# Performance work log

Measured on AMD Instinct MI355X. Metric: run time of the kernel, lower is better.

Reference implementation:

```python
import jax, jax.numpy as jnp
import numpy as np

DN = ('NCHW', 'OIHW', 'NCHW')

def conv(x, w, b, stride, pad):
    y = jax.lax.conv_general_dilated(x, w, (stride, stride), ((pad, pad), (pad, pad)), dimension_numbers=DN)
    return y + b[None, :, None, None]

def conv_transpose(x, w, b, stride, pad):
    # w has torch ConvTranspose2d layout (Cin, Cout, kh, kw)
    k = w.shape[2]
    w_f = jnp.transpose(w[:, :, ::-1, ::-1], (1, 0, 2, 3))  # -> OIHW, spatially flipped
    p = k - 1 - pad
    y = jax.lax.conv_general_dilated(x, w_f, (1, 1), ((p, p), (p, p)), lhs_dilation=(stride, stride), dimension_numbers=DN)
    return y + b[None, :, None, None]

def setup_inputs() -> dict:
    key = jax.random.key(0)
    ks = jax.random.split(key, 16)
    K, D = 512, 64
    s = 0.05
    inp = {
        'x': jax.random.uniform(ks[0], (32, 3, 256, 256), dtype=jnp.float32),
        'enc_w1': jax.random.normal(ks[1], (32, 3, 4, 4), jnp.float32) * s,
        'enc_b1': jnp.zeros((32,), jnp.float32),
        'enc_w2': jax.random.normal(ks[2], (64, 32, 4, 4), jnp.float32) * s,
        'enc_b2': jnp.zeros((64,), jnp.float32),
        'enc_w3': jax.random.normal(ks[3], (D, 64, 3, 3), jnp.float32) * s,
        'enc_b3': jnp.zeros((D,), jnp.float32),
        'codebook': jax.random.uniform(ks[4], (K, D), jnp.float32, -1.0 / K, 1.0 / K),
        'dec_w1': jax.random.normal(ks[5], (D, 64, 4, 4), jnp.float32) * s,   # ConvT (Cin,Cout,k,k)
        'dec_b1': jnp.zeros((64,), jnp.float32),
        'dec_w2': jax.random.normal(ks[6], (64, 32, 4, 4), jnp.float32) * s,  # ConvT
        'dec_b2': jnp.zeros((32,), jnp.float32),
        'dec_w3': jax.random.normal(ks[7], (3, 32, 3, 3), jnp.float32) * s,
        'dec_b3': jnp.zeros((3,), jnp.float32),
    }
    return inp

COMMITMENT_COST = 0.25

def reference(x, enc_w1, enc_b1, enc_w2, enc_b2, enc_w3, enc_b3, codebook,
              dec_w1, dec_b1, dec_w2, dec_b2, dec_w3, dec_b3):
    sg = jax.lax.stop_gradient
    # encoder
    h = jax.nn.relu(conv(x, enc_w1, enc_b1, 2, 1))
    h = jax.nn.relu(conv(h, enc_w2, enc_b2, 2, 1))
    z = conv(h, enc_w3, enc_b3, 1, 1)  # [B, D, H/4, W/4]
    # vector quantizer
    D = codebook.shape[1]
    z_perm = jnp.transpose(z, (0, 2, 3, 1))  # BHWD
    flat = z_perm.reshape(-1, D)  # [N, D]
    dist = jnp.sum(flat * flat, axis=1, keepdims=True) - 2.0 * (flat @ codebook.T) + jnp.sum(codebook * codebook, axis=1)  # [N, K]
    idx = jnp.argmin(dist, axis=1)
    q = codebook[idx].reshape(z_perm.shape)
    q = jnp.transpose(q, (0, 3, 1, 2))  # BDHW
    vq_loss = jnp.mean((sg(q) - z) ** 2) + COMMITMENT_COST * jnp.mean((q - sg(z)) ** 2)
    q_st = z + sg(q - z)  # straight-through
    # decoder
    h = jax.nn.relu(conv_transpose(q_st, dec_w1, dec_b1, 2, 1))
    h = jax.nn.relu(conv_transpose(h, dec_w2, dec_b2, 2, 1))
    recon = jax.nn.sigmoid(conv(h, dec_w3, dec_b3, 1, 1))
    return recon, vq_loss
```

## Files before the change

kernel.cpp:

```cpp
#include <hip/hip_runtime.h>

typedef unsigned short u16;
typedef unsigned int u32;
typedef __attribute__((ext_vector_type(8))) short bf16x8;
typedef __attribute__((ext_vector_type(4))) float f32x4;

#define MFMA(a, b, c) __builtin_amdgcn_mfma_f32_16x16x32_bf16(a, b, c, 0, 0, 0)

__device__ __forceinline__ float b2f(u32 lo16) {
  union { u32 i; float f; } v; v.i = lo16 << 16; return v.f;
}
__device__ __forceinline__ u16 f2b(float f) {
  union { float f; u32 i; } v; v.f = f;
  return (u16)((v.i + 0x7fffu + ((v.i >> 16) & 1u)) >> 16);
}
__device__ __forceinline__ u32 pk2(float a, float b) {
  u32 r; asm("v_cvt_pk_bf16_f32 %0, %1, %2" : "=v"(r) : "v"(a), "v"(b)); return r;
}
__device__ __forceinline__ bf16x8 ld8(const u16* p) { return *(const bf16x8*)p; }

__global__ void prep_k(const float* __restrict__ ew1, const float* __restrict__ ew2,
                       const float* __restrict__ ew3, const float* __restrict__ dw1,
                       const float* __restrict__ dw2, const float* __restrict__ dw3,
                       const float* __restrict__ cb,
                       float* W1, u16* Bp2, u16* Bp3, u16* BpT1, u16* BpT2,
                       u16* Bpd3, u16* Bpvq, float* cnorm, float* loss) {
  int tid = blockIdx.x * blockDim.x + threadIdx.x;
  int nth = gridDim.x * blockDim.x;
  for (int i = tid; i < 1536; i += nth) {
    int oc = i & 31; int r = i >> 5; int kw = r & 3; r >>= 2; int kh = r & 3; int ic = r >> 2;
    W1[i] = ew1[((oc*3 + ic)*4 + kh)*4 + kw];
  }
  for (int i = tid; i < 32768; i += nth) {
    int j = i & 7, li = (i >> 3) & 63, nt = (i >> 9) & 3, t = i >> 11;
    int ic = 8*(li >> 4) + j, oc = 16*nt + (li & 15), kh = t >> 2, kw = t & 3;
    Bp2[i] = f2b(ew2[((oc*32 + ic)*4 + kh)*4 + kw]);
  }
  for (int i = tid; i < 36864; i += nth) {
    int j = i & 7, li = (i >> 3) & 63, nt = (i >> 9) & 3, kc = (i >> 11) & 1, t = i >> 12;
    int ic = 32*kc + 8*(li >> 4) + j, oc = 16*nt + (li & 15), kh = t / 3, kw = t % 3;
    Bp3[i] = f2b(ew3[((oc*64 + ic)*3 + kh)*3 + kw]);
  }
  for (int i = tid; i < 65536; i += nth) {
    int j = i & 7, li = (i >> 3) & 63, nt = (i >> 9) & 3, kc = (i >> 11) & 1,
        t = (i >> 12) & 3, p = i >> 14;
    int a = p >> 1, b = p & 1;
    int ky = (1 - a) + 2*(t >> 1), kx = (1 - b) + 2*(t & 1);
    int ic = 32*kc + 8*(li >> 4) + j, oc = 16*nt + (li & 15);
    BpT1[i] = f2b(dw1[((ic*64 + oc)*4 + ky)*4 + kx]);
  }
  for (int i = tid; i < 32768; i += nth) {
    int j = i & 7, li = (i >> 3) & 63, mt = (i >> 9) & 1, kc = (i >> 10) & 1,
        t = (i >> 11) & 3, p = i >> 13;
    int a = p >> 1, b = p & 1;
    int ky = (1 - a) + 2*(t >> 1), kx = (1 - b) + 2*(t & 1);
    int oc = 16*mt + (li & 15);
    int ic = 32*kc + 8*(li >> 4) + j;
    BpT2[i] = f2b(dw2[((ic*32 + oc)*4 + ky)*4 + kx]);
  }
  for (int i = tid; i < 4608; i += nth) {
    int j = i & 7, li = (i >> 3) & 63, t = i >> 9;
    int n = li & 15, ic = 8*(li >> 4) + j, kh = t / 3, kw = t % 3;
    Bpd3[i] = (n < 3) ? f2b(dw3[((n*32 + ic)*3 + kh)*3 + kw]) : (u16)0;
  }
  for (int i = tid; i < 32768; i += nth) {
    int j = i & 7, li = (i >> 3) & 63, nt = (i >> 9) & 31, kc = i >> 14;
    int d = 32*kc + 8*(li >> 4) + j, code = 16*nt + (li & 15);
    Bpvq[i] = f2b(cb[code*64 + d]);
  }
  for (int k = tid; k < 512; k += nth) {
    float s = 0.f;
    for (int d = 0; d < 64; ++d) { float c = cb[k*64 + d]; s += c*c; }
    cnorm[k] = s;
  }
  if (tid == 0) *loss = 0.f;
}

__global__ __launch_bounds__(256) void conv1_k(
    const float* __restrict__ x, const float* __restrict__ W1,
    const float* __restrict__ b1, u16* __restrict__ h1) {
  __shared__ float ins[3*18*36];
  int Tx = blockIdx.x, Ty = blockIdx.y, b = blockIdx.z;
  int tid = threadIdx.x;
  for (int i = tid; i < 3*18*36; i += 256) {
    int c = i % 36; int r = (i / 36) % 18; int ic = i / 648;
    int iy = 16*Ty - 1 + r, ix = 32*Tx - 2 + c;
    float v = 0.f;
    if ((unsigned)iy < 256u && (unsigned)ix < 256u)
      v = x[((size_t)(b*3 + ic)*256 + iy)*256 + ix];
    ins[i] = v;
  }
  __syncthreads();
  int posg = tid & 31, ocg = tid >> 5;
  int Y = posg >> 2, Xg = posg & 3;
  int oc0 = ocg * 4;
  float acc[4][4];
#pragma unroll
  for (int j = 0; j < 4; ++j) { float bv = b1[oc0 + j];
#pragma unroll
    for (int e = 0; e < 4; ++e) acc[j][e] = bv; }
  for (int ic = 0; ic < 3; ++ic)
#pragma unroll
    for (int kh = 0; kh < 4; ++kh) {
      const float* row = &ins[ic*648 + (2*Y + kh)*36 + 8*Xg];
      float win[12];
#pragma unroll
      for (int t = 0; t < 12; ++t) win[t] = row[t];
#pragma unroll
      for (int kw = 0; kw < 4; ++kw) {
        const float* wp = &W1[((ic*4 + kh)*4 + kw)*32 + oc0];
        float w0 = wp[0], w1 = wp[1], w2 = wp[2], w3 = wp[3];
#pragma unroll
        for (int e = 0; e < 4; ++e) {
          float v = win[2*e + kw + 1];
          acc[0][e] += w0*v; acc[1][e] += w1*v; acc[2][e] += w2*v; acc[3][e] += w3*v;
        }
      }
    }
  int oy = 8*Ty + Y;
  int oxb = 16*Tx + 4*Xg;
#pragma unroll
  for (int e = 0; e < 4; ++e) {
    u32 lo = pk2(fmaxf(acc[0][e], 0.f), fmaxf(acc[1][e], 0.f));
    u32 hi = pk2(fmaxf(acc[2][e], 0.f), fmaxf(acc[3][e], 0.f));
    *(uint2*)&h1[((size_t)(b*128 + oy)*128 + oxb + e)*32 + oc0] = (uint2){lo, hi};
  }
}

__global__ __launch_bounds__(256) void conv2_k(
    const u16* __restrict__ h1, const u16* __restrict__ Bp2,
    const float* __restrict__ eb2, u16* __restrict__ h2) {
  __shared__ u16 lds[2448*8];
  int Tx = blockIdx.x, Ty = blockIdx.y, img = blockIdx.z;
  int tid = threadIdx.x;
  for (int i = tid; i < 2448; i += 256) {
    int c = i & 3; int x = (i >> 2) % 34; int row = (i >> 2) / 34;
    int iy = 16*Ty - 1 + row, ix = 32*Tx - 1 + x;
    f32x4 v = {0,0,0,0};
    if ((unsigned)iy < 128u && (unsigned)ix < 128u)
      v = *(const f32x4*)(h1 + (((size_t)(img*128 + iy)*128 + ix)*32 + c*8));
    *(f32x4*)(lds + ((row*4 + c)*34 + x)*8) = v;
  }
  __syncthreads();
  int w = tid >> 6, l = tid & 63, lg = l >> 4, lc = l & 15;
  f32x4 acc[2][4];
#pragma unroll
  for (int mt = 0; mt < 4; ++mt) {
    f32x4 bv = *(const f32x4*)(eb2 + mt*16 + 4*lg);
    acc[0][mt] = bv; acc[1][mt] = bv;
  }
#pragma unroll
  for (int t = 0; t < 16; ++t) {
    int kh = t >> 2, kw = t & 3;
    bf16x8 a0 = ld8(lds + (((2*w + kh)*4 + lg)*34 + 2*lc + kw)*8);
    bf16x8 a1 = ld8(lds + (((2*(w+4) + kh)*4 + lg)*34 + 2*lc + kw)*8);
    const u16* bp = Bp2 + t*2048 + l*8;
    bf16x8 w0 = ld8(bp), w1 = ld8(bp + 512), w2 = ld8(bp + 1024), w3 = ld8(bp + 1536);
    acc[0][0] = MFMA(w0, a0, acc[0][0]); acc[0][1] = MFMA(w1, a0, acc[0][1]);
    acc[0][2] = MFMA(w2, a0, acc[0][2]); acc[0][3] = MFMA(w3, a0, acc[0][3]);
    acc[1][0] = MFMA(w0, a1, acc[1][0]); acc[1][1] = MFMA(w1, a1, acc[1][1]);
    acc[1][2] = MFMA(w2, a1, acc[1][2]); acc[1][3] = MFMA(w3, a1, acc[1][3]);
  }
#pragma unroll
  for (int m = 0; m < 2; ++m) {
    int oy = 8*Ty + w + m*4;
    u16* base = h2 + ((size_t)(img*64 + oy)*64 + 16*Tx + lc)*64 + 4*lg;
#pragma unroll
    for (int mt = 0; mt < 4; ++mt) {
      f32x4 v = acc[m][mt];
      u32 lo = pk2(fmaxf(v[0], 0.f), fmaxf(v[1], 0.f));
      u32 hi = pk2(fmaxf(v[2], 0.f), fmaxf(v[3], 0.f));
      *(uint2*)(base + mt*16) = (uint2){lo, hi};
    }
  }
}

__global__ __launch_bounds__(256) void conv3e_k(
    const u16* __restrict__ h2, const u16* __restrict__ Bp3,
    const float* __restrict__ eb3, u16* __restrict__ z) {
  __shared__ u16 lds[1440*8];
  int Tx = blockIdx.x, Ty = blockIdx.y, img = blockIdx.z;
  int tid = threadIdx.x;
  for (int i = tid; i < 1440; i += 256) {
    int c = i & 7; int x = (i >> 3) % 18; int row = (i >> 3) / 18;
    int iy = 8*Ty - 1 + row, ix = 16*Tx - 1 + x;
    f32x4 v = {0,0,0,0};
    if ((unsigned)iy < 64u && (unsigned)ix < 64u)
      v = *(const f32x4*)(h2 + (((size_t)(img*64 + iy)*64 + ix)*64 + c*8));
    *(f32x4*)(lds + ((row*8 + c)*18 + x)*8) = v;
  }
  __syncthreads();
  int w = tid >> 6, l = tid & 63, lg = l >> 4, lc = l & 15;
  f32x4 acc[2][4];
#pragma unroll
  for (int mt = 0; mt < 4; ++mt) {
    f32x4 bv = *(const f32x4*)(eb3 + mt*16 + 4*lg);
    acc[0][mt] = bv; acc[1][mt] = bv;
  }
#pragma unroll
  for (int t = 0; t < 9; ++t) {
    int kh = t / 3, kw = t % 3;
#pragma unroll
    for (int kc = 0; kc < 2; ++kc) {
      bf16x8 a0 = ld8(lds + (((w + kh)*8 + kc*4 + lg)*18 + lc + kw)*8);
      bf16x8 a1 = ld8(lds + (((w + 4 + kh)*8 + kc*4 + lg)*18 + lc + kw)*8);
      const u16* bp = Bp3 + (t*2 + kc)*2048 + l*8;
      bf16x8 w0 = ld8(bp), w1 = ld8(bp + 512), w2 = ld8(bp + 1024), w3 = ld8(bp + 1536);
      acc[0][0] = MFMA(w0, a0, acc[0][0]); acc[0][1] = MFMA(w1, a0, acc[0][1]);
      acc[0][2] = MFMA(w2, a0, acc[0][2]); acc[0][3] = MFMA(w3, a0, acc[0][3]);
      acc[1][0] = MFMA(w0, a1, acc[1][0]); acc[1][1] = MFMA(w1, a1, acc[1][1]);
      acc[1][2] = MFMA(w2, a1, acc[1][2]); acc[1][3] = MFMA(w3, a1, acc[1][3]);
    }
  }
#pragma unroll
  for (int m = 0; m < 2; ++m) {
    int oy = 8*Ty + w + m*4;
    u16* base = z + ((size_t)(img*64 + oy)*64 + 16*Tx + lc)*64 + 4*lg;
#pragma unroll
    for (int mt = 0; mt < 4; ++mt) {
      f32x4 v = acc[m][mt];
      *(uint2*)(base + mt*16) = (uint2){pk2(v[0], v[1]), pk2(v[2], v[3])};
    }
  }
}

__global__ __launch_bounds__(256) void vqm_k(
    const u16* __restrict__ z, const u16* __restrict__ Bpvq,
    const float* __restrict__ cnorm, const float* __restrict__ cbf,
    u16* __restrict__ q, float* __restrict__ loss) {
  __shared__ u16 cbl[32768];
  __shared__ float cnl[512];
  __shared__ int idxl[64];
  __shared__ float red[256];
  int tid = threadIdx.x;
  for (int i = tid; i < 4096; i += 256)
    *(f32x4*)(cbl + i*8) = *(const f32x4*)(Bpvq + i*8);
  for (int i = tid; i < 512; i += 256) cnl[i] = cnorm[i];
  __syncthreads();
  int w = tid >> 6, l = tid & 63, lg = l >> 4, lc = l & 15;
  int wglobal = blockIdx.x*4 + w;
  float lsum = 0.f;
  for (int it = 0; it < 2; ++it) {
    int mf = wglobal + it*4096;
    size_t P = (size_t)mf * 16;
    bf16x8 a0 = ld8(z + (P + lc)*64 + lg*8);
    bf16x8 a1 = ld8(z + (P + lc)*64 + 32 + lg*8);
    float best[4] = {1e30f, 1e30f, 1e30f, 1e30f};
    int bidx[4] = {0, 0, 0, 0};
    for (int nt = 0; nt < 32; ++nt) {
      f32x4 acc = {0,0,0,0};
      acc = MFMA(a0, ld8(cbl + (nt*64 + l)*8), acc);
      acc = MFMA(a1, ld8(cbl + ((32 + nt)*64 + l)*8), acc);
      float cn = cnl[nt*16 + lc];
      int code = nt*16 + lc;
#pragma unroll
      for (int r = 0; r < 4; ++r) {
        float dist = cn - 2.f*acc[r];
        if (dist < best[r]) { best[r] = dist; bidx[r] = code; }
      }
    }
#pragma unroll
    for (int r = 0; r < 4; ++r) {
      float b = best[r]; int bi = bidx[r];
      for (int m = 1; m < 16; m <<= 1) {
        float ob = __shfl_xor(b, m);
        int oi = __shfl_xor(bi, m);
        if (ob < b || (ob == b && oi < bi)) { b = ob; bi = oi; }
      }
      if (lc == 0) idxl[w*16 + lg*4 + r] = bi;
    }
    int m = lc, ch0 = lg*16;
    int id = idxl[w*16 + m];
    const float* crow = cbf + (size_t)id*64 + ch0;
    const u16* zp = z + (P + m)*64 + ch0;
    u32* qp = (u32*)(q + (P + m)*64 + ch0);
#pragma unroll
    for (int c = 0; c < 16; c += 2) {
      float c0 = crow[c], c1 = crow[c+1];
      float d0 = c0 - b2f(zp[c]), d1 = c1 - b2f(zp[c+1]);
      lsum += d0*d0 + d1*d1;
      qp[c >> 1] = pk2(c0, c1);
    }
  }
  red[tid] = lsum;
  __syncthreads();
  for (int s = 128; s > 0; s >>= 1) {
    if (tid < s) red[tid] += red[tid + s];
    __syncthreads();
  }
  if (tid == 0) atomicAdd(loss, red[0] * (1.25f / 8388608.f));
}

__global__ __launch_bounds__(256) void convt1_k(
    const u16* __restrict__ q, const u16* __restrict__ BpT1,
    const float* __restrict__ db1, u16* __restrict__ d1) {
  __shared__ u16 lds[864*8];
  int Tx = blockIdx.x, Ty = blockIdx.y, img = blockIdx.z;
  int X0 = 16*Tx, P0 = 4*Ty;
  int tid = threadIdx.x;
  for (int i = tid; i < 864; i += 256) {
    int c = i & 7; int x = (i >> 3) % 18; int row = (i >> 3) / 18;
    int iy = P0 - 1 + row, ix = X0 - 1 + x;
    f32x4 v = {0,0,0,0};
    if ((unsigned)iy < 64u && (unsigned)ix < 64u)
      v = *(const f32x4*)(q + (((size_t)(img*64 + iy)*64 + ix)*64 + c*8));
    *(f32x4*)(lds + ((row*8 + c)*18 + x)*8) = v;
  }
  __syncthreads();
  int w = tid >> 6, l = tid & 63, lg = l >> 4, lc = l & 15;
  int a = w & 1, bp_ = w >> 1;
  f32x4 acc[4][4];
#pragma unroll
  for (int mt = 0; mt < 4; ++mt) {
    f32x4 bv = *(const f32x4*)(db1 + mt*16 + 4*lg);
#pragma unroll
    for (int m = 0; m < 4; ++m) acc[m][mt] = bv;
  }
  const u16* bbase = BpT1 + (size_t)(a*2 + bp_)*16384;
#pragma unroll
  for (int t = 0; t < 4; ++t) {
    int kyi = t >> 1, kxi = t & 1;
#pragma unroll
    for (int kc = 0; kc < 2; ++kc) {
      const u16* bp = bbase + (t*2 + kc)*2048 + l*8;
      bf16x8 w0 = ld8(bp), w1 = ld8(bp + 512), w2 = ld8(bp + 1024), w3 = ld8(bp + 1536);
      int xg = lc + bp_ - kxi + 1;
#pragma unroll
      for (int m = 0; m < 4; ++m) {
        int rowg = m + a - kyi + 1;
        bf16x8 dv = ld8(lds + ((rowg*8 + kc*4 + lg)*18 + xg)*8);
        acc[m][0] = MFMA(w0, dv, acc[m][0]);
        acc[m][1] = MFMA(w1, dv, acc[m][1]);
        acc[m][2] = MFMA(w2, dv, acc[m][2]);
        acc[m][3] = MFMA(w3, dv, acc[m][3]);
      }
    }
  }
  int ox = 2*(X0 + lc) + bp_;
#pragma unroll
  for (int m = 0; m < 4; ++m) {
    int oy = 2*(P0 + m) + a;
    u16* base = d1 + ((size_t)(img*128 + oy)*128 + ox)*64 + 4*lg;
#pragma unroll
    for (int mt = 0; mt < 4; ++mt) {
      f32x4 v = acc[m][mt];
      u32 lo = pk2(fmaxf(v[0], 0.f), fmaxf(v[1], 0.f));
      u32 hi = pk2(fmaxf(v[2], 0.f), fmaxf(v[3], 0.f));
      *(uint2*)(base + mt*16) = (uint2){lo, hi};
    }
  }
}

__global__ __launch_bounds__(256) void tail_k(
    const u16* __restrict__ d1, const u16* __restrict__ BpT2,
    const float* __restrict__ db2, const u16* __restrict__ Bpd3,
    const float* __restrict__ db3, float* __restrict__ out) {
  __shared__ u16 d1s[680*8];
  __shared__ u16 d2q[10240];
  int Tx = blockIdx.x, Ty = blockIdx.y, img = blockIdx.z;
  int DX0 = 30*Tx - 1, DY0 = 6*Ty - 1;
  int IYB = 3*Ty, IXB = 15*Tx;
  int tid = threadIdx.x;
  bool edge = (Tx == 0) | (Tx == 8) | (Ty == 0) | (Ty == 42);
  for (int i = tid; i < 680; i += 256) {
    int x = i % 17; int rc = i / 17; int c = rc & 7; int row = rc >> 3;
    int iy = IYB - 1 + row, ix = IXB - 1 + x;
    f32x4 v = {0,0,0,0};
    if ((unsigned)iy < 128u && (unsigned)ix < 128u)
      v = *(const f32x4*)(d1 + (((size_t)(img*128 + iy)*128 + ix)*64 + c*8));
    *(f32x4*)(d1s + ((row*8 + c)*17 + x)*8) = v;
  }
  __syncthreads();
  int w = tid >> 6, l = tid & 63, lg = l >> 4, lc = l & 15;
  {
    int a = w & 1, b = w >> 1;
    f32x4 acc[4][2];
#pragma unroll
    for (int mt = 0; mt < 2; ++mt) {
      f32x4 bv = *(const f32x4*)(db2 + 16*mt + 4*lg);
#pragma unroll
      for (int m = 0; m < 4; ++m) acc[m][mt] = bv;
    }
    const u16* bbase = BpT2 + (size_t)(a*2 + b)*8192;
#pragma unroll
    for (int kxi = 0; kxi < 2; ++kxi) {
      int xg = lc - kxi + 1;
#pragma unroll
      for (int kc = 0; kc < 2; ++kc) {
        bf16x8 av[5];
#pragma unroll
        for (int rr = 0; rr < 5; ++rr)
          av[rr] = ld8(d1s + ((rr*8 + kc*4 + lg)*17 + xg)*8);
#pragma unroll
        for (int kyi = 0; kyi < 2; ++kyi) {
          int t = kyi*2 + kxi;
          const u16* wb = bbase + (t*2 + kc)*1024 + l*8;
          bf16x8 w0 = ld8(wb), w1 = ld8(wb + 512);
#pragma unroll
          for (int m = 0; m < 4; ++m) {
            acc[m][0] = MFMA(w0, av[m + 1 - kyi], acc[m][0]);
            acc[m][1] = MFMA(w1, av[m + 1 - kyi], acc[m][1]);
          }
        }
      }
    }
    int base = (a*2 + b)*2560 + lc*40 + 4*lg;
    if (!edge) {
#pragma unroll
      for (int m = 0; m < 4; ++m)
#pragma unroll
        for (int mt = 0; mt < 2; ++mt) {
          f32x4 v = acc[m][mt];
          u32 lo = pk2(fmaxf(v[0], 0.f), fmaxf(v[1], 0.f));
          u32 hi = pk2(fmaxf(v[2], 0.f), fmaxf(v[3], 0.f));
          *(uint2*)(d2q + base + m*640 + mt*16) = (uint2){lo, hi};
        }
    } else {
      int oxc = b ? DX0 : DX0 + 1;
      bool cm = (unsigned)(oxc + 2*lc) < 256u;
      int oyc = a ? DY0 : DY0 + 1;
#pragma unroll
      for (int m = 0; m < 4; ++m) {
        bool ok = ((unsigned)(oyc + 2*m) < 256u) && cm;
#pragma unroll
        for (int mt = 0; mt < 2; ++mt) {
          f32x4 v = acc[m][mt];
          u32 lo = 0, hi = 0;
          if (ok) {
            lo = pk2(fmaxf(v[0], 0.f), fmaxf(v[1], 0.f));
            hi = pk2(fmaxf(v[2], 0.f), fmaxf(v[3], 0.f));
          }
          *(uint2*)(d2q + base + m*640 + mt*16) = (uint2){lo, hi};
        }
      }
    }
  }
  __syncthreads();
  bf16x8 bw[9];
#pragma unroll
  for (int t = 0; t < 9; ++t) bw[t] = ld8(Bpd3 + t*512 + l*8);
  float bv3 = (lc < 3) ? db3[lc] : 0.f;
#pragma unroll
  for (int i = 0; i < 3; ++i) {
    int u = w + 4*i;
    int yy = u >> 1, xf = u & 1;
    int gy = DY0 + 1 + yy;
    int cOff[3];
#pragma unroll
    for (int kw = 0; kw < 3; ++kw) {
      int lx = xf*16 + lc + kw; if (lx > 31) lx = 31;
      cOff[kw] = (1 - (lx & 1))*2560 + (lx >> 1)*40 + 8*lg;
    }
    f32x4 acc = {bv3, bv3, bv3, bv3};
#pragma unroll
    for (int kh = 0; kh < 3; ++kh) {
      int ly = yy + kh;
      int rOff = (1 - (ly & 1))*5120 + (ly >> 1)*640;
#pragma unroll
      for (int kw = 0; kw < 3; ++kw)
        acc = MFMA(ld8(d2q + rOff + cOff[kw]), bw[kh*3 + kw], acc);
    }
    if (lc < 3) {
      if (!edge) {
#pragma unroll
        for (int r = 0; r < 4; ++r) {
          int xi = xf*16 + 4*lg + r;
          if (xi < 30)
            out[((size_t)(img*3 + lc)*256 + gy)*256 + DX0 + 1 + xi] =
                __builtin_amdgcn_rcpf(1.f + __expf(-acc[r]));
        }
      } else if ((unsigned)gy < 256u) {
#pragma unroll
        for (int r = 0; r < 4; ++r) {
          int xi = xf*16 + 4*lg + r;
          int gx = DX0 + 1 + xi;
          if (xi < 30 && (unsigned)gx < 256u)
            out[((size_t)(img*3 + lc)*256 + gy)*256 + gx] =
                __builtin_amdgcn_rcpf(1.f + __expf(-acc[r]));
        }
      }
    }
  }
}

extern "C" void kernel_launch(void* const* d_in, const int* in_sizes, int n_in,
                              void* d_out, int out_size, void* d_ws, size_t ws_size,
                              hipStream_t stream) {
  const float* x   = (const float*)d_in[0];
  const float* ew1 = (const float*)d_in[1];
  const float* eb1 = (const float*)d_in[2];
  const float* ew2 = (const float*)d_in[3];
  const float* eb2 = (const float*)d_in[4];
  const float* ew3 = (const float*)d_in[5];
  const float* eb3 = (const float*)d_in[6];
  const float* cb  = (const float*)d_in[7];
  const float* dw1 = (const float*)d_in[8];
  const float* db1 = (const float*)d_in[9];
  const float* dw2 = (const float*)d_in[10];
  const float* db2 = (const float*)d_in[11];
  const float* dw3 = (const float*)d_in[12];
  const float* db3 = (const float*)d_in[13];
  float* out = (float*)d_out;

  char* ws = (char*)d_ws;
  const size_t MB = 1048576;
  u16* h1 = (u16*)ws;
  u16* q  = (u16*)ws;
  u16* d1 = (u16*)(ws + 16*MB);
  u16* h2 = (u16*)(ws + 32*MB);
  u16* z  = (u16*)(ws + 48*MB);
  char* wp = ws + 80*MB;
  float* W1   = (float*)wp;  wp += 6144;
  u16*  Bp2   = (u16*)wp;    wp += 65536;
  u16*  Bp3   = (u16*)wp;    wp += 73728;
  u16*  BpT1  = (u16*)wp;    wp += 131072;
  u16*  BpT2  = (u16*)wp;    wp += 65536;
  u16*  Bpd3  = (u16*)wp;    wp += 9216;
  u16*  Bpvq  = (u16*)wp;    wp += 65536;
  float* cnorm = (float*)wp; wp += 2048;
  float* loss = out + 6291456;

  prep_k<<<64, 256, 0, stream>>>(ew1, ew2, ew3, dw1, dw2, dw3, cb,
                                 W1, Bp2, Bp3, BpT1, BpT2, Bpd3, Bpvq, cnorm, loss);
  conv1_k<<<dim3(8, 16, 32), 256, 0, stream>>>(x, W1, eb1, h1);
  conv2_k<<<dim3(4, 8, 32), 256, 0, stream>>>(h1, Bp2, eb2, h2);
  conv3e_k<<<dim3(4, 8, 32), 256, 0, stream>>>(h2, Bp3, eb3, z);
  vqm_k<<<1024, 256, 0, stream>>>(z, Bpvq, cnorm, cb, q, loss);
  convt1_k<<<dim3(4, 16, 32), 256, 0, stream>>>(q, BpT1, db1, d1);
  tail_k<<<dim3(9, 43, 32), 256, 0, stream>>>(d1, BpT2, db2, Bpd3, db3, out);
}
```

Before: 298.9 us.

## Store intermediates in zero-padded layouts and read conv inputs directly from global

After: 393.2 us. 31.6% more time.

```diff
diff --git a/kernel.cpp b/kernel.cpp
--- a/kernel.cpp
+++ b/kernel.cpp
@@ -18,13 +18,15 @@
   u32 r; asm("v_cvt_pk_bf16_f32 %0, %1, %2" : "=v"(r) : "v"(a), "v"(b)); return r;
 }
 __device__ __forceinline__ bf16x8 ld8(const u16* p) { return *(const bf16x8*)p; }
+
 
 __global__ void prep_k(const float* __restrict__ ew1, const float* __restrict__ ew2,
                        const float* __restrict__ ew3, const float* __restrict__ dw1,
                        const float* __restrict__ dw2, const float* __restrict__ dw3,
                        const float* __restrict__ cb,
                        float* W1, u16* Bp2, u16* Bp3, u16* BpT1, u16* BpT2,
-                       u16* Bpd3, u16* Bpvq, float* cnorm, float* loss) {
+                       u16* Bpd3, u16* Bpvq, float* cnorm, float* loss,
+                       u16* h2p, u16* qp) {
   int tid = blockIdx.x * blockDim.x + threadIdx.x;
   int nth = gridDim.x * blockDim.x;
   for (int i = tid; i < 1536; i += nth) {
@@ -73,7 +75,33 @@
     for (int d = 0; d < 64; ++d) { float c = cb[k*64 + d]; s += c*c; }
     cnorm[k] = s;
   }
+  for (int i = tid; i < 32*260; i += nth) {
+    int im = i / 260, c = i % 260;
+    int y, x;
+    if (c < 66) { y = 0; x = c; }
+    else if (c < 132) { y = 65; x = c - 66; }
+    else if (c < 196) { y = c - 131; x = 0; }
+    else { y = c - 195; x = 65; }
+    size_t off = ((size_t)(im*66 + y)*66 + x)*64;
+    uint4 zv = {0,0,0,0};
+    uint4* p1 = (uint4*)(h2p + off); uint4* p2 = (uint4*)(qp + off);
+#pragma unroll
+    for (int j = 0; j < 8; ++j) { p1[j] = zv; p2[j] = zv; }
+  }
   if (tid == 0) *loss = 0.f;
+}
+
+__global__ void zpad_k(u16* __restrict__ d1p) {
+  int i = blockIdx.x*256 + threadIdx.x;
+  if (i >= 32*2624) return;
+  int im = i / 2624, c = i % 2624;
+  int row, col;
+  if (c < 576) { int rr = c / 144; row = (rr == 0) ? 0 : 128 + rr; col = c % 144; }
+  else { int c2 = c - 576; row = c2 / 16 + 1; int k = c2 & 15; col = k ? 128 + k : 0; }
+  uint4* p = (uint4*)(d1p + ((size_t)(im*132 + row)*144 + col)*64);
+  uint4 zv = {0,0,0,0};
+#pragma unroll
+  for (int j = 0; j < 8; ++j) p[j] = zv;
 }
 
 __global__ __launch_bounds__(256) void conv1_k(
@@ -129,7 +157,7 @@
 
 __global__ __launch_bounds__(256) void conv2_k(
     const u16* __restrict__ h1, const u16* __restrict__ Bp2,
-    const float* __restrict__ eb2, u16* __restrict__ h2) {
+    const float* __restrict__ eb2, u16* __restrict__ h2p) {
   __shared__ u16 lds[2448*8];
   int Tx = blockIdx.x, Ty = blockIdx.y, img = blockIdx.z;
   int tid = threadIdx.x;
@@ -164,7 +192,7 @@
 #pragma unroll
   for (int m = 0; m < 2; ++m) {
     int oy = 8*Ty + w + m*4;
-    u16* base = h2 + ((size_t)(img*64 + oy)*64 + 16*Tx + lc)*64 + 4*lg;
+    u16* base = h2p + (((size_t)img*66 + oy + 1)*66 + 16*Tx + lc + 1)*64 + 4*lg;
 #pragma unroll
     for (int mt = 0; mt < 4; ++mt) {
       f32x4 v = acc[m][mt];
@@ -176,21 +204,14 @@
 }
 
 __global__ __launch_bounds__(256) void conv3e_k(
-    const u16* __restrict__ h2, const u16* __restrict__ Bp3,
+    const u16* __restrict__ h2p, const u16* __restrict__ Bp3,
     const float* __restrict__ eb3, u16* __restrict__ z) {
-  __shared__ u16 lds[1440*8];
   int Tx = blockIdx.x, Ty = blockIdx.y, img = blockIdx.z;
   int tid = threadIdx.x;
-  for (int i = tid; i < 1440; i += 256) {
-    int c = i & 7; int x = (i >> 3) % 18; int row = (i >> 3) / 18;
-    int iy = 8*Ty - 1 + row, ix = 16*Tx - 1 + x;
-    f32x4 v = {0,0,0,0};
-    if ((unsigned)iy < 64u && (unsigned)ix < 64u)
-      v = *(const f32x4*)(h2 + (((size_t)(img*64 + iy)*64 + ix)*64 + c*8));
-    *(f32x4*)(lds + ((row*8 + c)*18 + x)*8) = v;
-  }
-  __syncthreads();
   int w = tid >> 6, l = tid & 63, lg = l >> 4, lc = l & 15;
+  const u16* hbase = h2p + (size_t)img * (66*66*64);
+  int row0 = 8*Ty + w;
+  int col = 16*Tx + lc;
   f32x4 acc[2][4];
 #pragma unroll
   for (int mt = 0; mt < 4; ++mt) {
@@ -202,8 +223,8 @@
     int kh = t / 3, kw = t % 3;
 #pragma unroll
     for (int kc = 0; kc < 2; ++kc) {
-      bf16x8 a0 = ld8(lds + (((w + kh)*8 + kc*4 + lg)*18 + lc + kw)*8);
-      bf16x8 a1 = ld8(lds + (((w + 4 + kh)*8 + kc*4 + lg)*18 + lc + kw)*8);
+      bf16x8 a0 = ld8(hbase + ((size_t)(row0 + kh)*66 + col + kw)*64 + kc*32 + lg*8);
+      bf16x8 a1 = ld8(hbase + ((size_t)(row0 + 4 + kh)*66 + col + kw)*64 + kc*32 + lg*8);
       const u16* bp = Bp3 + (t*2 + kc)*2048 + l*8;
       bf16x8 w0 = ld8(bp), w1 = ld8(bp + 512), w2 = ld8(bp + 1024), w3 = ld8(bp + 1536);
       acc[0][0] = MFMA(w0, a0, acc[0][0]); acc[0][1] = MFMA(w1, a0, acc[0][1]);
@@ -227,7 +248,7 @@
 __global__ __launch_bounds__(256) void vqm_k(
     const u16* __restrict__ z, const u16* __restrict__ Bpvq,
     const float* __restrict__ cnorm, const float* __restrict__ cbf,
-    u16* __restrict__ q, float* __restrict__ loss) {
+    u16* __restrict__ qp, float* __restrict__ loss) {
   __shared__ u16 cbl[32768];
   __shared__ float cnl[512];
   __shared__ int idxl[64];
@@ -273,13 +294,15 @@
     int id = idxl[w*16 + m];
     const float* crow = cbf + (size_t)id*64 + ch0;
     const u16* zp = z + (P + m)*64 + ch0;
-    u32* qp = (u32*)(q + (P + m)*64 + ch0);
+    int n = (int)P + m;
+    int im2 = n >> 12, hw2 = n & 4095, yy2 = hw2 >> 6, xx2 = hw2 & 63;
+    u32* qpw = (u32*)(qp + ((size_t)(im2*66 + yy2 + 1)*66 + xx2 + 1)*64 + ch0);
 #pragma unroll
     for (int c = 0; c < 16; c += 2) {
       float c0 = crow[c], c1 = crow[c+1];
       float d0 = c0 - b2f(zp[c]), d1 = c1 - b2f(zp[c+1]);
       lsum += d0*d0 + d1*d1;
-      qp[c >> 1] = pk2(c0, c1);
+      qpw[c >> 1] = pk2(c0, c1);
     }
   }
   red[tid] = lsum;
@@ -292,23 +315,14 @@
 }
 
 __global__ __launch_bounds__(256) void convt1_k(
-    const u16* __restrict__ q, const u16* __restrict__ BpT1,
-    const float* __restrict__ db1, u16* __restrict__ d1) {
-  __shared__ u16 lds[864*8];
+    const u16* __restrict__ qp, const u16* __restrict__ BpT1,
+    const float* __restrict__ db1, u16* __restrict__ d1p) {
   int Tx = blockIdx.x, Ty = blockIdx.y, img = blockIdx.z;
   int X0 = 16*Tx, P0 = 4*Ty;
   int tid = threadIdx.x;
-  for (int i = tid; i < 864; i += 256) {
-    int c = i & 7; int x = (i >> 3) % 18; int row = (i >> 3) / 18;
-    int iy = P0 - 1 + row, ix = X0 - 1 + x;
-    f32x4 v = {0,0,0,0};
-    if ((unsigned)iy < 64u && (unsigned)ix < 64u)
-      v = *(const f32x4*)(q + (((size_t)(img*64 + iy)*64 + ix)*64 + c*8));
-    *(f32x4*)(lds + ((row*8 + c)*18 + x)*8) = v;
-  }
-  __syncthreads();
   int w = tid >> 6, l = tid & 63, lg = l >> 4, lc = l & 15;
   int a = w & 1, bp_ = w >> 1;
+  const u16* qbase = qp + (size_t)img * (66*66*64);
   f32x4 acc[4][4];
 #pragma unroll
   for (int mt = 0; mt < 4; ++mt) {
@@ -318,21 +332,27 @@
   }
   const u16* bbase = BpT1 + (size_t)(a*2 + bp_)*16384;
 #pragma unroll
-  for (int t = 0; t < 4; ++t) {
-    int kyi = t >> 1, kxi = t & 1;
+  for (int kxi = 0; kxi < 2; ++kxi) {
+    int colp = X0 + 1 + lc + bp_ - kxi;
 #pragma unroll
     for (int kc = 0; kc < 2; ++kc) {
-      const u16* bp = bbase + (t*2 + kc)*2048 + l*8;
-      bf16x8 w0 = ld8(bp), w1 = ld8(bp + 512), w2 = ld8(bp + 1024), w3 = ld8(bp + 1536);
-      int xg = lc + bp_ - kxi + 1;
-#pragma unroll
-      for (int m = 0; m < 4; ++m) {
-        int rowg = m + a - kyi + 1;
-        bf16x8 dv = ld8(lds + ((rowg*8 + kc*4 + lg)*18 + xg)*8);
-        acc[m][0] = MFMA(w0, dv, acc[m][0]);
-        acc[m][1] = MFMA(w1, dv, acc[m][1]);
-        acc[m][2] = MFMA(w2, dv, acc[m][2]);
-        acc[m][3] = MFMA(w3, dv, acc[m][3]);
+      bf16x8 av[5];
+#pragma unroll
+      for (int rr = 0; rr < 5; ++rr)
+        av[rr] = ld8(qbase + ((size_t)(P0 + rr)*66 + colp)*64 + kc*32 + lg*8);
+#pragma unroll
+      for (int kyi = 0; kyi < 2; ++kyi) {
+        int t = kyi*2 + kxi;
+        const u16* bp = bbase + (t*2 + kc)*2048 + l*8;
+        bf16x8 w0 = ld8(bp), w1 = ld8(bp + 512), w2 = ld8(bp + 1024), w3 = ld8(bp + 1536);
+#pragma unroll
+        for (int m = 0; m < 4; ++m) {
+          bf16x8 dv = av[m + 1 - kyi];
+          acc[m][0] = MFMA(w0, dv, acc[m][0]);
+          acc[m][1] = MFMA(w1, dv, acc[m][1]);
+          acc[m][2] = MFMA(w2, dv, acc[m][2]);
+          acc[m][3] = MFMA(w3, dv, acc[m][3]);
+        }
       }
     }
   }
@@ -340,7 +360,7 @@
 #pragma unroll
   for (int m = 0; m < 4; ++m) {
     int oy = 2*(P0 + m) + a;
-    u16* base = d1 + ((size_t)(img*128 + oy)*128 + ox)*64 + 4*lg;
+    u16* base = d1p + ((size_t)(img*132 + oy + 1)*144 + ox + 1)*64 + 4*lg;
 #pragma unroll
     for (int mt = 0; mt < 4; ++mt) {
       f32x4 v = acc[m][mt];
@@ -352,26 +372,17 @@
 }
 
 __global__ __launch_bounds__(256) void tail_k(
-    const u16* __restrict__ d1, const u16* __restrict__ BpT2,
+    const u16* __restrict__ d1p, const u16* __restrict__ BpT2,
     const float* __restrict__ db2, const u16* __restrict__ Bpd3,
     const float* __restrict__ db3, float* __restrict__ out) {
-  __shared__ u16 d1s[680*8];
   __shared__ u16 d2q[10240];
   int Tx = blockIdx.x, Ty = blockIdx.y, img = blockIdx.z;
   int DX0 = 30*Tx - 1, DY0 = 6*Ty - 1;
   int IYB = 3*Ty, IXB = 15*Tx;
   int tid = threadIdx.x;
   bool edge = (Tx == 0) | (Tx == 8) | (Ty == 0) | (Ty == 42);
-  for (int i = tid; i < 680; i += 256) {
-    int x = i % 17; int rc = i / 17; int c = rc & 7; int row = rc >> 3;
-    int iy = IYB - 1 + row, ix = IXB - 1 + x;
-    f32x4 v = {0,0,0,0};
-    if ((unsigned)iy < 128u && (unsigned)ix < 128u)
-      v = *(const f32x4*)(d1 + (((size_t)(img*128 + iy)*128 + ix)*64 + c*8));
-    *(f32x4*)(d1s + ((row*8 + c)*17 + x)*8) = v;
-  }
-  __syncthreads();
   int w = tid >> 6, l = tid & 63, lg = l >> 4, lc = l & 15;
+  const u16* dbase = d1p + (size_t)img * (132*144*64);
   {
     int a = w & 1, b = w >> 1;
     f32x4 acc[4][2];
@@ -384,13 +395,13 @@
     const u16* bbase = BpT2 + (size_t)(a*2 + b)*8192;
 #pragma unroll
     for (int kxi = 0; kxi < 2; ++kxi) {
-      int xg = lc - kxi + 1;
+      int colp = IXB + lc - kxi + 1;
 #pragma unroll
       for (int kc = 0; kc < 2; ++kc) {
         bf16x8 av[5];
 #pragma unroll
         for (int rr = 0; rr < 5; ++rr)
-          av[rr] = ld8(d1s + ((rr*8 + kc*4 + lg)*17 + xg)*8);
+          av[rr] = ld8(dbase + ((size_t)(IYB + rr)*144 + colp)*64 + kc*32 + lg*8);
 #pragma unroll
         for (int kyi = 0; kyi < 2; ++kyi) {
           int t = kyi*2 + kxi;
@@ -504,12 +515,12 @@
 
   char* ws = (char*)d_ws;
   const size_t MB = 1048576;
-  u16* h1 = (u16*)ws;
-  u16* q  = (u16*)ws;
-  u16* d1 = (u16*)(ws + 16*MB);
-  u16* h2 = (u16*)(ws + 32*MB);
-  u16* z  = (u16*)(ws + 48*MB);
-  char* wp = ws + 80*MB;
+  u16* d1p = (u16*)ws;
+  u16* z   = (u16*)ws;
+  u16* h2p = (u16*)(ws + 17*MB);
+  u16* h1  = (u16*)(ws + 35*MB);
+  u16* qp  = (u16*)(ws + 78*MB);
+  char* wp = ws + 96*MB;
   float* W1   = (float*)wp;  wp += 6144;
   u16*  Bp2   = (u16*)wp;    wp += 65536;
   u16*  Bp3   = (u16*)wp;    wp += 73728;
@@ -521,11 +532,13 @@
   float* loss = out + 6291456;
 
   prep_k<<<64, 256, 0, stream>>>(ew1, ew2, ew3, dw1, dw2, dw3, cb,
-                                 W1, Bp2, Bp3, BpT1, BpT2, Bpd3, Bpvq, cnorm, loss);
+                                 W1, Bp2, Bp3, BpT1, BpT2, Bpd3, Bpvq, cnorm, loss,
+                                 h2p, qp);
   conv1_k<<<dim3(8, 16, 32), 256, 0, stream>>>(x, W1, eb1, h1);
-  conv2_k<<<dim3(4, 8, 32), 256, 0, stream>>>(h1, Bp2, eb2, h2);
-  conv3e_k<<<dim3(4, 8, 32), 256, 0, stream>>>(h2, Bp3, eb3, z);
-  vqm_k<<<1024, 256, 0, stream>>>(z, Bpvq, cnorm, cb, q, loss);
-  convt1_k<<<dim3(4, 16, 32), 256, 0, stream>>>(q, BpT1, db1, d1);
-  tail_k<<<dim3(9, 43, 32), 256, 0, stream>>>(d1, BpT2, db2, Bpd3, db3, out);
-}
+  conv2_k<<<dim3(4, 8, 32), 256, 0, stream>>>(h1, Bp2, eb2, h2p);
+  conv3e_k<<<dim3(4, 8, 32), 256, 0, stream>>>(h2p, Bp3, eb3, z);
+  vqm_k<<<1024, 256, 0, stream>>>(z, Bpvq, cnorm, cb, qp, loss);
+  zpad_k<<<328, 256, 0, stream>>>(d1p);
+  convt1_k<<<dim3(4, 16, 32), 256, 0, stream>>>(qp, BpT1, db1, d1p);
+  tail_k<<<dim3(9, 43, 32), 256, 0, stream>>>(d1p, BpT2, db2, Bpd3, db3, out);
+}
```
